# Optimization experiments

Hardware: AMD Instinct MI355X
Metric: run time of the kernel (lower is better)

The kernel has to match this reference:

```python
import jax, jax.numpy as jnp
import numpy as np

T, B, IN_DIM, MEM_DIM = 256, 64, 512, 512


def _kaiming(key, shape):
    # kaiming_normal_ default: fan_in = shape[1], gain = sqrt(2)
    std = np.sqrt(2.0 / shape[1])
    return jax.random.normal(key, shape, dtype=jnp.float32) * std


def setup_inputs() -> dict:
    key = jax.random.key(0)
    ks = jax.random.split(key, 10)
    inp = {
        "inputs": jax.random.normal(ks[0], (T, B, IN_DIM), dtype=jnp.float32),
        "emb_s": jax.random.normal(ks[1], (T, B, IN_DIM), dtype=jnp.float32),
        "c0": jnp.zeros((B, MEM_DIM), dtype=jnp.float32),
        "h0": jnp.zeros((B, MEM_DIM), dtype=jnp.float32),
        # learned params (torch Linear: y = x @ W.T + b)
        "W_ioux": _kaiming(ks[2], (4 * MEM_DIM, IN_DIM)),
        "b_ioux": jnp.zeros((4 * MEM_DIM,), jnp.float32),
        "W_iouh": _kaiming(ks[3], (4 * MEM_DIM, MEM_DIM)),
        "b_iouh": jnp.zeros((4 * MEM_DIM,), jnp.float32),
        "W_ious": _kaiming(ks[4], (4 * MEM_DIM, IN_DIM)),
        "b_ious": jnp.zeros((4 * MEM_DIM,), jnp.float32),
        "W_fx": _kaiming(ks[5], (MEM_DIM, IN_DIM)),
        "b_fx": jnp.zeros((MEM_DIM,), jnp.float32),
        "W_fh": _kaiming(ks[6], (MEM_DIM, MEM_DIM)),
        "b_fh": jnp.zeros((MEM_DIM,), jnp.float32),
        "W_wc": _kaiming(ks[7], (MEM_DIM, IN_DIM)),
        "b_wc": jnp.zeros((MEM_DIM,), jnp.float32),
    }
    return inp


def reference(inputs, emb_s, c0, h0,
              W_ioux, b_ioux, W_iouh, b_iouh, W_ious, b_ious,
              W_fx, b_fx, W_fh, b_fh, W_wc, b_wc):
    M = W_fh.shape[0]
    # Precompute all input-dependent projections for the whole sequence (big GEMMs).
    iou_x = (jnp.einsum('tbi,gi->tbg', inputs, W_ioux) + b_ioux
             + jnp.einsum('tbi,gi->tbg', emb_s, W_ious) + b_ious)      # [T,B,4M]
    ctelta_x = jnp.einsum('tbi,mi->tbm', inputs, W_fx) + b_fx          # [T,B,M]
    wc_s = jnp.tanh(jnp.einsum('tbi,mi->tbm', emb_s, W_wc) + b_wc)    # [T,B,M]

    def step(carry, xs):
        c, h = carry
        iou_t, ctx_t, wcs_t = xs
        iou = iou_t + h @ W_iouh.T + b_iouh                            # [B,4M]
        f, i, o, o_c = jnp.split(jax.nn.sigmoid(iou), 4, axis=1)
        c_telta = jnp.tanh(ctx_t + h @ W_fh.T + b_fh)
        c_new = i * c_telta + f * c
        h_new = o * jnp.tanh(c_new) + o_c * wcs_t
        return (c_new, h_new), h_new

    (c_fin, h_fin), out = jax.lax.scan(step, (c0, h0), (iou_x, ctelta_x, wc_s))
    return out, (c_fin, h_fin)
```

## Files before the change

### kernel.cpp

```cpp
#include <hip/hip_runtime.h>
#include <stdint.h>

#define T_STEPS 256
#define B_DIM   64
#define MDIM    512
#define NROWS   (T_STEPS * B_DIM)
#define KCAT    1024
#define NBIG    3072
#define W2ROWS  2560
#define NBLK2   32
#define OUT_N   ((size_t)T_STEPS * B_DIM * MDIM)

typedef short v8s __attribute__((ext_vector_type(8)));
typedef float v4f __attribute__((ext_vector_type(4)));
typedef unsigned long long u64;

static __device__ __forceinline__ unsigned short f2bf(float f) {
    unsigned u = __builtin_bit_cast(unsigned, f);
    u += 0x7FFFu + ((u >> 16) & 1u);
    return (unsigned short)(u >> 16);
}
static __device__ __forceinline__ float bf2f(unsigned short h) {
    unsigned u = ((unsigned)h) << 16;
    return __builtin_bit_cast(float, u);
}
static __device__ __forceinline__ float fast_rcp(float x) {
    return __builtin_amdgcn_rcpf(x);
}
static __device__ __forceinline__ float sigmoid_fast(float x) {
    return fast_rcp(1.0f + __expf(-x));
}
static __device__ __forceinline__ float tanh_fast(float x) {
    return 1.0f - 2.0f * fast_rcp(1.0f + __expf(2.0f * x));
}


__global__ void pack_xcat(const float* __restrict__ x, const float* __restrict__ s,
                          unsigned short* __restrict__ xcat) {
    int idx = blockIdx.x * blockDim.x + threadIdx.x;
    if (idx >= NROWS * KCAT) return;
    int row = idx >> 10, col = idx & 1023;
    float v = (col < 512) ? x[row * 512 + col] : s[row * 512 + (col - 512)];
    xcat[idx] = f2bf(v);
}

__global__ void pack_wbig(const float* __restrict__ Wioux, const float* __restrict__ bioux,
                          const float* __restrict__ Wious, const float* __restrict__ bious,
                          const float* __restrict__ Wfx,   const float* __restrict__ bfx,
                          const float* __restrict__ Wwc,   const float* __restrict__ bwc,
                          unsigned short* __restrict__ wbig, float* __restrict__ bbig) {
    int idx = blockIdx.x * blockDim.x + threadIdx.x;
    if (idx >= NBIG * KCAT) return;
    int r = idx >> 10, c = idx & 1023;
    float v;
    if (r < 2048)      v = (c < 512) ? Wioux[r * 512 + c] : Wious[r * 512 + (c - 512)];
    else if (r < 2560) { int j = r - 2048; v = (c < 512) ? Wfx[j * 512 + c] : 0.0f; }
    else               { int j = r - 2560; v = (c < 512) ? 0.0f : Wwc[j * 512 + (c - 512)]; }
    wbig[idx] = f2bf(v);
    if (c == 0) {
        float b;
        if (r < 2048)      b = bioux[r] + bious[r];
        else if (r < 2560) b = bfx[r - 2048];
        else               b = bwc[r - 2560];
        bbig[r] = b;
    }
}

__global__ void pack_w2(const float* __restrict__ Wiouh, const float* __restrict__ biouh,
                        const float* __restrict__ Wfh,   const float* __restrict__ bfh,
                        unsigned short* __restrict__ w2, float* __restrict__ b2) {
    int idx = blockIdx.x * blockDim.x + threadIdx.x;
    if (idx >= W2ROWS * 512) return;
    int r = idx >> 9, k = idx & 511;
    int bk = r / 80, rem = r % 80, g = rem >> 4, j = rem & 15;
    int m = bk * 16 + j;
    float v, bias;
    if (g < 4) { v = Wiouh[(size_t)(g * 512 + m) * 512 + k]; bias = biouh[g * 512 + m]; }
    else       { v = Wfh[(size_t)m * 512 + k];               bias = bfh[m]; }
    w2[idx] = f2bf(v);
    if (k == 0) b2[r] = bias;
}

__global__ void init_state(const float* __restrict__ h0,
                           unsigned short* __restrict__ hslab0,
                           int* __restrict__ flags) {
    int idx = blockIdx.x * blockDim.x + threadIdx.x;
    if (idx < 2048) flags[idx] = 0;
    if (idx >= B_DIM * MDIM) return;
    int row = idx >> 9, col = idx & 511;
    hslab0[((col >> 4) * 64 + row) * 16 + (col & 15)] = f2bf(h0[idx]);
}


__global__ __launch_bounds__(256) void gemm_big(
        const unsigned short* __restrict__ xcat,
        const unsigned short* __restrict__ wbig,
        const float* __restrict__ bbig,
        unsigned short* __restrict__ ytile) {
    __shared__ __align__(16) unsigned short As[128][40];
    __shared__ __align__(16) unsigned short Bs[128][40];
    int nb = blockIdx.x;
    int mb = blockIdx.y;
    int tid = threadIdx.x;
    int lane = tid & 63, wid = tid >> 6;
    int wm = wid & 1, wn = wid >> 1;
    int lm = lane & 15, lq = lane >> 4;
    v4f acc[4][4] = {};
    for (int kb = 0; kb < KCAT / 32; ++kb) {
        __syncthreads();
        #pragma unroll
        for (int it = 0; it < 2; ++it) {
            int cid = tid + it * 256;
            int r = cid >> 2, q = cid & 3;
            *(uint4*)&As[r][q * 8] =
                *(const uint4*)(xcat + (size_t)(mb * 128 + r) * KCAT + kb * 32 + q * 8);
            *(uint4*)&Bs[r][q * 8] =
                *(const uint4*)(wbig + (size_t)(nb * 128 + r) * KCAT + kb * 32 + q * 8);
        }
        __syncthreads();
        v8s a[4], b[4];
        #pragma unroll
        for (int i = 0; i < 4; ++i) a[i] = *(const v8s*)&As[wm * 64 + i * 16 + lm][lq * 8];
        #pragma unroll
        for (int j = 0; j < 4; ++j) b[j] = *(const v8s*)&Bs[wn * 64 + j * 16 + lm][lq * 8];
        #pragma unroll
        for (int i = 0; i < 4; ++i)
            #pragma unroll
            for (int j = 0; j < 4; ++j)
                acc[i][j] = __builtin_amdgcn_mfma_f32_16x16x32_bf16(a[i], b[j], acc[i][j], 0, 0, 0);
    }
    int tt = mb * 2 + wm;
    #pragma unroll
    for (int i = 0; i < 4; ++i) {
        int rbase = i * 16 + lq * 4;
        #pragma unroll
        for (int j = 0; j < 4; ++j) {
            int gn = nb * 128 + wn * 64 + j * 16 + lm;
            float bias = bbig[gn];
            bool do_tanh = (gn >= 2560);
            int slot, mcol;
            if (gn < 2048)      { slot = gn >> 9; mcol = gn & 511; }
            else if (gn < 2560) { slot = 4; mcol = gn - 2048; }
            else                { slot = 5; mcol = gn - 2560; }
            size_t base = ((((size_t)tt * NBLK2 + (mcol >> 4)) * 64 + rbase) * 6 + slot) * 16
                          + (mcol & 15);
            #pragma unroll
            for (int r = 0; r < 4; ++r) {
                float v = acc[i][j][r] + bias;
                if (do_tanh) v = tanhf(v);
                ytile[base + (size_t)r * 96] = f2bf(v);
            }
        }
    }
}


__global__ __launch_bounds__(256, 1) void lstm_persist(
        const unsigned short* __restrict__ ytile,
        const unsigned short* __restrict__ w2,
        const float* __restrict__ b2,
        const float* __restrict__ c0,
        unsigned short* hslab0,
        unsigned short* hslab1,
        float* __restrict__ out,
        int* __restrict__ flags) {
    __shared__ __align__(16) float red[2][10][256];
    __shared__ __align__(16) unsigned short ybuf[2][6144];
    int bk = blockIdx.x;
    int tid = threadIdx.x;
    int lane = tid & 63, wid = tid >> 6;
    int p = wid >> 1;
    int q = wid & 1;
    int lm = lane & 15, lq = lane >> 4;
    int m = bk * 16 + lm;

    v8s bfrag[5][8];
    const unsigned short* w2b = w2 + (size_t)(bk * 80 + lm) * 512 + lq * 8;
    #pragma unroll
    for (int g = 0; g < 5; ++g)
        #pragma unroll
        for (int j = 0; j < 8; ++j)
            bfrag[g][j] = *(const v8s*)(w2b + (size_t)g * 16 * 512 + (q * 8 + j) * 32);

    float bias[5];
    #pragma unroll
    for (int g = 0; g < 5; ++g) bias[g] = b2[(bk * 5 + g) * 16 + lm];
    float creg[2][4];
    #pragma unroll
    for (int tb = 0; tb < 2; ++tb)
        #pragma unroll
        for (int r = 0; r < 4; ++r)
            creg[tb][r] = c0[(p * 32 + tb * 16 + lq * 4 + r) * 512 + m];

    if (q == 1) {
        const unsigned short* slab = ytile + (size_t)bk * 6144;
        #pragma unroll
        for (int i = 0; i < 6; ++i) {
            int ch = p * 6 + i;
            __builtin_amdgcn_global_load_lds(
                (const __attribute__((address_space(1))) unsigned int*)(slab + ch * 512 + lane * 8),
                (__attribute__((address_space(3))) unsigned int*)(&ybuf[0][0] + ch * 512), 16, 0, 0);
        }
    }

    for (int t = 0; t < T_STEPS; ++t) {
        int cur = t & 1;
        if (t) {
            if (wid == 1)
                while (!__all(__hip_atomic_load(flags + lane * 32, __ATOMIC_RELAXED,
                                                __HIP_MEMORY_SCOPE_AGENT) >= t)) {}
            __syncthreads();
            asm volatile("" ::: "memory");
        }
        const u64* hin = cur ? (const u64*)hslab1 : (const u64*)hslab0;
        unsigned*  hnx = cur ? (unsigned*)hslab0 : (unsigned*)hslab1;
        u64 hq[32];
        {
            const u64* hb = hin + ((size_t)(q * 16 + (lq >> 1)) * 64 + p * 32 + lm) * 4
                          + (lq & 1) * 2;
            #pragma unroll
            for (int j = 0; j < 8; ++j) {
                hq[j * 4 + 0] = __hip_atomic_load(hb + j * 512,      __ATOMIC_RELAXED, __HIP_MEMORY_SCOPE_AGENT);
                hq[j * 4 + 1] = __hip_atomic_load(hb + j * 512 + 1,  __ATOMIC_RELAXED, __HIP_MEMORY_SCOPE_AGENT);
                hq[j * 4 + 2] = __hip_atomic_load(hb + j * 512 + 64, __ATOMIC_RELAXED, __HIP_MEMORY_SCOPE_AGENT);
                hq[j * 4 + 3] = __hip_atomic_load(hb + j * 512 + 65, __ATOMIC_RELAXED, __HIP_MEMORY_SCOPE_AGENT);
            }
        }
        v4f acc[2][5] = {};
        #pragma unroll
        for (int j = 0; j < 8; ++j) {
            union { u64 qq[2]; v8s v; } a0, a1;
            a0.qq[0] = hq[j * 4 + 0]; a0.qq[1] = hq[j * 4 + 1];
            a1.qq[0] = hq[j * 4 + 2]; a1.qq[1] = hq[j * 4 + 3];
            #pragma unroll
            for (int g = 0; g < 5; ++g) {
                acc[0][g] = __builtin_amdgcn_mfma_f32_16x16x32_bf16(a0.v, bfrag[g][j], acc[0][g], 0, 0, 0);
                acc[1][g] = __builtin_amdgcn_mfma_f32_16x16x32_bf16(a1.v, bfrag[g][j], acc[1][g], 0, 0, 0);
            }
        }
        if (q == 1) {
            #pragma unroll
            for (int tb = 0; tb < 2; ++tb)
                #pragma unroll
                for (int g = 0; g < 5; ++g)
                    *(v4f*)&red[p][tb * 5 + g][lane * 4] = acc[tb][g];
        }
        __syncthreads();
        if (q == 0) {
            #pragma unroll
            for (int tb = 0; tb < 2; ++tb)
                #pragma unroll
                for (int g = 0; g < 5; ++g)
                    acc[tb][g] += *(const v4f*)&red[p][tb * 5 + g][lane * 4];
            const unsigned short* yb = &ybuf[cur][0];
            float hnv[2][4];
            unsigned hbf[2][4];
            #pragma unroll
            for (int tb = 0; tb < 2; ++tb) {
                #pragma unroll
                for (int r = 0; r < 4; ++r) {
                    int brow = p * 32 + tb * 16 + lq * 4 + r;
                    const unsigned short* ybr = yb + brow * 96;
                    float f_ = sigmoid_fast(bf2f(ybr[0 * 16 + lm]) + acc[tb][0][r] + bias[0]);
                    float i_ = sigmoid_fast(bf2f(ybr[1 * 16 + lm]) + acc[tb][1][r] + bias[1]);
                    float o_ = sigmoid_fast(bf2f(ybr[2 * 16 + lm]) + acc[tb][2][r] + bias[2]);
                    float oc = sigmoid_fast(bf2f(ybr[3 * 16 + lm]) + acc[tb][3][r] + bias[3]);
                    float ct = tanh_fast  (bf2f(ybr[4 * 16 + lm]) + acc[tb][4][r] + bias[4]);
                    float wcs = bf2f(ybr[5 * 16 + lm]);
                    float cn = i_ * ct + f_ * creg[tb][r];
                    creg[tb][r] = cn;
                    float hn = o_ * tanh_fast(cn) + oc * wcs;
                    hnv[tb][r] = hn;
                    hbf[tb][r] = f2bf(hn);
                }
            }
            #pragma unroll
            for (int tb = 0; tb < 2; ++tb)
                #pragma unroll
                for (int r = 0; r < 4; ++r) {
                    int brow = p * 32 + tb * 16 + lq * 4 + r;
                    unsigned other = (unsigned)__shfl_xor((int)hbf[tb][r], 1);
                    if ((lm & 1) == 0) {
                        unsigned w = (hbf[tb][r] & 0xFFFFu) | (other << 16);
                        __hip_atomic_store(hnx + (size_t)(bk * 64 + brow) * 8 + (lm >> 1), w,
                                           __ATOMIC_RELAXED, __HIP_MEMORY_SCOPE_AGENT);
                    }
                }
            asm volatile("s_waitcnt vmcnt(0)" ::: "memory");
            if (lane == 0 && t + 1 < T_STEPS)
                __hip_atomic_store(flags + (bk * 2 + p) * 32, t + 1,
                                   __ATOMIC_RELAXED, __HIP_MEMORY_SCOPE_AGENT);
            #pragma unroll
            for (int tb = 0; tb < 2; ++tb)
                #pragma unroll
                for (int r = 0; r < 4; ++r) {
                    int brow = p * 32 + tb * 16 + lq * 4 + r;
                    out[((size_t)t * 64 + brow) * 512 + m] = hnv[tb][r];
                    if (t == T_STEPS - 1)
                        out[OUT_N + 32768 + (size_t)brow * 512 + m] = hnv[tb][r];
                }
        } else if (t + 1 < T_STEPS) {
            const unsigned short* slab = ytile + (size_t)((t + 1) * NBLK2 + bk) * 6144;
            unsigned short* lbase = &ybuf[cur ^ 1][0];
            #pragma unroll
            for (int i = 0; i < 6; ++i) {
                int ch = p * 6 + i;
                __builtin_amdgcn_global_load_lds(
                    (const __attribute__((address_space(1))) unsigned int*)(slab + ch * 512 + lane * 8),
                    (__attribute__((address_space(3))) unsigned int*)(lbase + ch * 512), 16, 0, 0);
            }
        }
    }

    if (q == 0) {
        #pragma unroll
        for (int tb = 0; tb < 2; ++tb)
            #pragma unroll
            for (int r = 0; r < 4; ++r)
                out[OUT_N + (size_t)(p * 32 + tb * 16 + lq * 4 + r) * 512 + m] = creg[tb][r];
    }
}


extern "C" void kernel_launch(void* const* d_in, const int* in_sizes, int n_in,
                              void* d_out, int out_size, void* d_ws, size_t ws_size,
                              hipStream_t stream) {
    const float* inputs = (const float*)d_in[0];
    const float* emb_s  = (const float*)d_in[1];
    const float* c0     = (const float*)d_in[2];
    const float* h0     = (const float*)d_in[3];
    const float* W_ioux = (const float*)d_in[4];  const float* b_ioux = (const float*)d_in[5];
    const float* W_iouh = (const float*)d_in[6];  const float* b_iouh = (const float*)d_in[7];
    const float* W_ious = (const float*)d_in[8];  const float* b_ious = (const float*)d_in[9];
    const float* W_fx   = (const float*)d_in[10]; const float* b_fx   = (const float*)d_in[11];
    const float* W_fh   = (const float*)d_in[12]; const float* b_fh   = (const float*)d_in[13];
    const float* W_wc   = (const float*)d_in[14]; const float* b_wc   = (const float*)d_in[15];
    float* out = (float*)d_out;

    char* ws = (char*)d_ws;
    size_t off = 0;
    auto alloc = [&](size_t bytes) -> void* {
        void* p = ws + off;
        off += (bytes + 255) & ~(size_t)255;
        return p;
    };
    unsigned short* ytile = (unsigned short*)alloc((size_t)NROWS * NBIG * 2);
    unsigned short* xcat  = (unsigned short*)alloc((size_t)NROWS * KCAT * 2);
    unsigned short* wbig  = (unsigned short*)alloc((size_t)NBIG * KCAT * 2);
    float*          bbig  = (float*)alloc(NBIG * 4);
    unsigned short* w2    = (unsigned short*)alloc((size_t)W2ROWS * 512 * 2);
    float*          b2    = (float*)alloc(W2ROWS * 4);
    unsigned short* hslab0 = (unsigned short*)alloc(B_DIM * MDIM * 2);
    unsigned short* hslab1 = (unsigned short*)alloc(B_DIM * MDIM * 2);
    int*            flags  = (int*)alloc(8192);

    pack_xcat<<<(NROWS * KCAT + 255) / 256, 256, 0, stream>>>(inputs, emb_s, xcat);
    pack_wbig<<<(NBIG * KCAT + 255) / 256, 256, 0, stream>>>(
        W_ioux, b_ioux, W_ious, b_ious, W_fx, b_fx, W_wc, b_wc, wbig, bbig);
    pack_w2<<<(W2ROWS * 512 + 255) / 256, 256, 0, stream>>>(W_iouh, b_iouh, W_fh, b_fh, w2, b2);
    init_state<<<(B_DIM * MDIM + 255) / 256, 256, 0, stream>>>(h0, hslab0, flags);

    dim3 g1(NBIG / 128, NROWS / 128);
    gemm_big<<<g1, 256, 0, stream>>>(xcat, wbig, bbig, ytile);

    lstm_persist<<<NBLK2, 256, 0, stream>>>(ytile, w2, b2, c0, hslab0, hslab1, out, flags);
}
```

Measured before the change: 1.884 ms.

## Replace flag barrier with per-element step tags on hidden-state words

The persistent LSTM kernel drops the separate flag array and spin barrier. Each hidden-state value is now stored as a 32-bit word carrying a bf16 value plus a step tag, and readers spin until every word they need carries the expected tag, so data and readiness arrive together. It also splits the gate epilogue across both wave halves instead of one, and uses a triple-buffered prefetch issued by all waves. The cost is twice the hidden-state traffic, repeated polling of 64 words per lane, and extra permute instructions to unpack the tagged words.

```diff
diff --git a/kernel.cpp b/kernel.cpp
--- a/kernel.cpp
+++ b/kernel.cpp
@@ -82,13 +82,12 @@
 }
 
 __global__ void init_state(const float* __restrict__ h0,
-                           unsigned short* __restrict__ hslab0,
-                           int* __restrict__ flags) {
+                           unsigned* __restrict__ hs0,
+                           unsigned* __restrict__ hs1) {
     int idx = blockIdx.x * blockDim.x + threadIdx.x;
-    if (idx < 2048) flags[idx] = 0;
     if (idx >= B_DIM * MDIM) return;
-    int row = idx >> 9, col = idx & 511;
-    hslab0[((col >> 4) * 64 + row) * 16 + (col & 15)] = f2bf(h0[idx]);
+    hs0[idx] = (unsigned)f2bf(h0[idx]);
+    hs1[idx] = 0xFFFF0000u;
 }
 
 
@@ -160,12 +159,11 @@
         const unsigned short* __restrict__ w2,
         const float* __restrict__ b2,
         const float* __restrict__ c0,
-        unsigned short* hslab0,
-        unsigned short* hslab1,
-        float* __restrict__ out,
-        int* __restrict__ flags) {
-    __shared__ __align__(16) float red[2][10][256];
-    __shared__ __align__(16) unsigned short ybuf[2][6144];
+        unsigned* hs0,
+        unsigned* hs1,
+        float* __restrict__ out) {
+    __shared__ __align__(16) float red[2][2][5][256];
+    __shared__ __align__(16) unsigned short ybuf[3][6144];
     int bk = blockIdx.x;
     int tid = threadIdx.x;
     int lane = tid & 63, wid = tid >> 6;
@@ -185,140 +183,112 @@
     float bias[5];
     #pragma unroll
     for (int g = 0; g < 5; ++g) bias[g] = b2[(bk * 5 + g) * 16 + lm];
-    float creg[2][4];
-    #pragma unroll
-    for (int tb = 0; tb < 2; ++tb)
-        #pragma unroll
-        for (int r = 0; r < 4; ++r)
-            creg[tb][r] = c0[(p * 32 + tb * 16 + lq * 4 + r) * 512 + m];
-
-    if (q == 1) {
-        const unsigned short* slab = ytile + (size_t)bk * 6144;
-        #pragma unroll
-        for (int i = 0; i < 6; ++i) {
-            int ch = p * 6 + i;
+    float creg[4];
+    #pragma unroll
+    for (int r = 0; r < 4; ++r)
+        creg[r] = c0[(p * 32 + q * 16 + lq * 4 + r) * 512 + m];
+
+    auto prefetch = [&](int tt, int buf) {
+        const unsigned short* slab = ytile + ((size_t)tt * NBLK2 + bk) * 6144;
+        unsigned short* lbase = &ybuf[buf][0];
+        #pragma unroll
+        for (int i = 0; i < 3; ++i) {
+            int ch = wid * 3 + i;
             __builtin_amdgcn_global_load_lds(
                 (const __attribute__((address_space(1))) unsigned int*)(slab + ch * 512 + lane * 8),
-                (__attribute__((address_space(3))) unsigned int*)(&ybuf[0][0] + ch * 512), 16, 0, 0);
-        }
-    }
+                (__attribute__((address_space(3))) unsigned int*)(lbase + ch * 512), 16, 0, 0);
+        }
+    };
+    prefetch(0, 0);
+    prefetch(1, 1);
 
     for (int t = 0; t < T_STEPS; ++t) {
-        int cur = t & 1;
-        if (t) {
-            if (wid == 1)
-                while (!__all(__hip_atomic_load(flags + lane * 32, __ATOMIC_RELAXED,
-                                                __HIP_MEMORY_SCOPE_AGENT) >= t)) {}
-            __syncthreads();
-            asm volatile("" ::: "memory");
-        }
-        const u64* hin = cur ? (const u64*)hslab1 : (const u64*)hslab0;
-        unsigned*  hnx = cur ? (unsigned*)hslab0 : (unsigned*)hslab1;
-        u64 hq[32];
+        const unsigned* hin = (t & 1) ? hs1 : hs0;
+        unsigned*       hnx = (t & 1) ? hs0 : hs1;
+        u64 wv[64];
         {
-            const u64* hb = hin + ((size_t)(q * 16 + (lq >> 1)) * 64 + p * 32 + lm) * 4
-                          + (lq & 1) * 2;
+            const u64* hb = (const u64*)hin + ((size_t)(p * 32 + lm)) * 256 + q * 128 + lq * 4;
+            unsigned tg = (unsigned)t & 0xFFFFu;
+            u64 ex = ((u64)tg << 16) | ((u64)tg << 48);
+            while (true) {
+                #pragma unroll
+                for (int j = 0; j < 8; ++j)
+                    #pragma unroll
+                    for (int e = 0; e < 4; ++e) {
+                        wv[j * 4 + e]      = __hip_atomic_load(hb + j * 16 + e,
+                                                __ATOMIC_RELAXED, __HIP_MEMORY_SCOPE_AGENT);
+                        wv[32 + j * 4 + e] = __hip_atomic_load(hb + 4096 + j * 16 + e,
+                                                __ATOMIC_RELAXED, __HIP_MEMORY_SCOPE_AGENT);
+                    }
+                bool ok = true;
+                #pragma unroll
+                for (int i = 0; i < 64; ++i)
+                    ok &= ((wv[i] & 0xFFFF0000FFFF0000ULL) == ex);
+                if (__all(ok)) break;
+            }
+        }
+        v8s a0[8], a1[8];
+        #pragma unroll
+        for (int j = 0; j < 8; ++j) {
+            union { unsigned u[4]; v8s v; } f0, f1;
             #pragma unroll
-            for (int j = 0; j < 8; ++j) {
-                hq[j * 4 + 0] = __hip_atomic_load(hb + j * 512,      __ATOMIC_RELAXED, __HIP_MEMORY_SCOPE_AGENT);
-                hq[j * 4 + 1] = __hip_atomic_load(hb + j * 512 + 1,  __ATOMIC_RELAXED, __HIP_MEMORY_SCOPE_AGENT);
-                hq[j * 4 + 2] = __hip_atomic_load(hb + j * 512 + 64, __ATOMIC_RELAXED, __HIP_MEMORY_SCOPE_AGENT);
-                hq[j * 4 + 3] = __hip_atomic_load(hb + j * 512 + 65, __ATOMIC_RELAXED, __HIP_MEMORY_SCOPE_AGENT);
+            for (int e = 0; e < 4; ++e) {
+                u64 x0 = wv[j * 4 + e], x1 = wv[32 + j * 4 + e];
+                f0.u[e] = __builtin_amdgcn_perm((unsigned)(x0 >> 32), (unsigned)x0, 0x05040100u);
+                f1.u[e] = __builtin_amdgcn_perm((unsigned)(x1 >> 32), (unsigned)x1, 0x05040100u);
             }
+            a0[j] = f0.v; a1[j] = f1.v;
         }
         v4f acc[2][5] = {};
         #pragma unroll
         for (int j = 0; j < 8; ++j) {
-            union { u64 qq[2]; v8s v; } a0, a1;
-            a0.qq[0] = hq[j * 4 + 0]; a0.qq[1] = hq[j * 4 + 1];
-            a1.qq[0] = hq[j * 4 + 2]; a1.qq[1] = hq[j * 4 + 3];
             #pragma unroll
             for (int g = 0; g < 5; ++g) {
-                acc[0][g] = __builtin_amdgcn_mfma_f32_16x16x32_bf16(a0.v, bfrag[g][j], acc[0][g], 0, 0, 0);
-                acc[1][g] = __builtin_amdgcn_mfma_f32_16x16x32_bf16(a1.v, bfrag[g][j], acc[1][g], 0, 0, 0);
+                acc[0][g] = __builtin_amdgcn_mfma_f32_16x16x32_bf16(a0[j], bfrag[g][j], acc[0][g], 0, 0, 0);
+                acc[1][g] = __builtin_amdgcn_mfma_f32_16x16x32_bf16(a1[j], bfrag[g][j], acc[1][g], 0, 0, 0);
             }
         }
-        if (q == 1) {
-            #pragma unroll
-            for (int tb = 0; tb < 2; ++tb)
-                #pragma unroll
-                for (int g = 0; g < 5; ++g)
-                    *(v4f*)&red[p][tb * 5 + g][lane * 4] = acc[tb][g];
-        }
+        #pragma unroll
+        for (int g = 0; g < 5; ++g)
+            *(v4f*)&red[p][q ^ 1][g][lane * 4] = acc[q ^ 1][g];
         __syncthreads();
-        if (q == 0) {
-            #pragma unroll
-            for (int tb = 0; tb < 2; ++tb)
-                #pragma unroll
-                for (int g = 0; g < 5; ++g)
-                    acc[tb][g] += *(const v4f*)&red[p][tb * 5 + g][lane * 4];
-            const unsigned short* yb = &ybuf[cur][0];
-            float hnv[2][4];
-            unsigned hbf[2][4];
-            #pragma unroll
-            for (int tb = 0; tb < 2; ++tb) {
-                #pragma unroll
-                for (int r = 0; r < 4; ++r) {
-                    int brow = p * 32 + tb * 16 + lq * 4 + r;
-                    const unsigned short* ybr = yb + brow * 96;
-                    float f_ = sigmoid_fast(bf2f(ybr[0 * 16 + lm]) + acc[tb][0][r] + bias[0]);
-                    float i_ = sigmoid_fast(bf2f(ybr[1 * 16 + lm]) + acc[tb][1][r] + bias[1]);
-                    float o_ = sigmoid_fast(bf2f(ybr[2 * 16 + lm]) + acc[tb][2][r] + bias[2]);
-                    float oc = sigmoid_fast(bf2f(ybr[3 * 16 + lm]) + acc[tb][3][r] + bias[3]);
-                    float ct = tanh_fast  (bf2f(ybr[4 * 16 + lm]) + acc[tb][4][r] + bias[4]);
-                    float wcs = bf2f(ybr[5 * 16 + lm]);
-                    float cn = i_ * ct + f_ * creg[tb][r];
-                    creg[tb][r] = cn;
-                    float hn = o_ * tanh_fast(cn) + oc * wcs;
-                    hnv[tb][r] = hn;
-                    hbf[tb][r] = f2bf(hn);
-                }
-            }
-            #pragma unroll
-            for (int tb = 0; tb < 2; ++tb)
-                #pragma unroll
-                for (int r = 0; r < 4; ++r) {
-                    int brow = p * 32 + tb * 16 + lq * 4 + r;
-                    unsigned other = (unsigned)__shfl_xor((int)hbf[tb][r], 1);
-                    if ((lm & 1) == 0) {
-                        unsigned w = (hbf[tb][r] & 0xFFFFu) | (other << 16);
-                        __hip_atomic_store(hnx + (size_t)(bk * 64 + brow) * 8 + (lm >> 1), w,
-                                           __ATOMIC_RELAXED, __HIP_MEMORY_SCOPE_AGENT);
-                    }
-                }
-            asm volatile("s_waitcnt vmcnt(0)" ::: "memory");
-            if (lane == 0 && t + 1 < T_STEPS)
-                __hip_atomic_store(flags + (bk * 2 + p) * 32, t + 1,
-                                   __ATOMIC_RELAXED, __HIP_MEMORY_SCOPE_AGENT);
-            #pragma unroll
-            for (int tb = 0; tb < 2; ++tb)
-                #pragma unroll
-                for (int r = 0; r < 4; ++r) {
-                    int brow = p * 32 + tb * 16 + lq * 4 + r;
-                    out[((size_t)t * 64 + brow) * 512 + m] = hnv[tb][r];
-                    if (t == T_STEPS - 1)
-                        out[OUT_N + 32768 + (size_t)brow * 512 + m] = hnv[tb][r];
-                }
-        } else if (t + 1 < T_STEPS) {
-            const unsigned short* slab = ytile + (size_t)((t + 1) * NBLK2 + bk) * 6144;
-            unsigned short* lbase = &ybuf[cur ^ 1][0];
-            #pragma unroll
-            for (int i = 0; i < 6; ++i) {
-                int ch = p * 6 + i;
-                __builtin_amdgcn_global_load_lds(
-                    (const __attribute__((address_space(1))) unsigned int*)(slab + ch * 512 + lane * 8),
-                    (__attribute__((address_space(3))) unsigned int*)(lbase + ch * 512), 16, 0, 0);
-            }
+        if (t + 2 < T_STEPS) prefetch(t + 2, (t + 2) % 3);
+        v4f fin[5];
+        #pragma unroll
+        for (int g = 0; g < 5; ++g)
+            fin[g] = acc[q][g] + *(const v4f*)&red[p][q][g][lane * 4];
+        const unsigned short* yb = &ybuf[t % 3][0];
+        unsigned tagup = ((unsigned)(t + 1)) << 16;
+        float hv[4];
+        #pragma unroll
+        for (int r = 0; r < 4; ++r) {
+            int brow = p * 32 + q * 16 + lq * 4 + r;
+            const unsigned short* ybr = yb + brow * 96;
+            float f_ = sigmoid_fast(bf2f(ybr[0 * 16 + lm]) + fin[0][r] + bias[0]);
+            float i_ = sigmoid_fast(bf2f(ybr[1 * 16 + lm]) + fin[1][r] + bias[1]);
+            float o_ = sigmoid_fast(bf2f(ybr[2 * 16 + lm]) + fin[2][r] + bias[2]);
+            float oc = sigmoid_fast(bf2f(ybr[3 * 16 + lm]) + fin[3][r] + bias[3]);
+            float ct = tanh_fast  (bf2f(ybr[4 * 16 + lm]) + fin[4][r] + bias[4]);
+            float wcs = bf2f(ybr[5 * 16 + lm]);
+            float cn = i_ * ct + f_ * creg[r];
+            creg[r] = cn;
+            float hn = o_ * tanh_fast(cn) + oc * wcs;
+            hv[r] = hn;
+            __hip_atomic_store(hnx + (size_t)brow * 512 + m, tagup | (unsigned)f2bf(hn),
+                               __ATOMIC_RELAXED, __HIP_MEMORY_SCOPE_AGENT);
+        }
+        #pragma unroll
+        for (int r = 0; r < 4; ++r) {
+            int brow = p * 32 + q * 16 + lq * 4 + r;
+            out[((size_t)t * 64 + brow) * 512 + m] = hv[r];
+            if (t == T_STEPS - 1)
+                out[OUT_N + 32768 + (size_t)brow * 512 + m] = hv[r];
         }
     }
 
-    if (q == 0) {
-        #pragma unroll
-        for (int tb = 0; tb < 2; ++tb)
-            #pragma unroll
-            for (int r = 0; r < 4; ++r)
-                out[OUT_N + (size_t)(p * 32 + tb * 16 + lq * 4 + r) * 512 + m] = creg[tb][r];
-    }
+    #pragma unroll
+    for (int r = 0; r < 4; ++r)
+        out[OUT_N + (size_t)(p * 32 + q * 16 + lq * 4 + r) * 512 + m] = creg[r];
 }
 
 
@@ -350,18 +320,17 @@
     float*          bbig  = (float*)alloc(NBIG * 4);
     unsigned short* w2    = (unsigned short*)alloc((size_t)W2ROWS * 512 * 2);
     float*          b2    = (float*)alloc(W2ROWS * 4);
-    unsigned short* hslab0 = (unsigned short*)alloc(B_DIM * MDIM * 2);
-    unsigned short* hslab1 = (unsigned short*)alloc(B_DIM * MDIM * 2);
-    int*            flags  = (int*)alloc(8192);
+    unsigned*       hs0   = (unsigned*)alloc((size_t)B_DIM * MDIM * 4);
+    unsigned*       hs1   = (unsigned*)alloc((size_t)B_DIM * MDIM * 4);
 
     pack_xcat<<<(NROWS * KCAT + 255) / 256, 256, 0, stream>>>(inputs, emb_s, xcat);
     pack_wbig<<<(NBIG * KCAT + 255) / 256, 256, 0, stream>>>(
         W_ioux, b_ioux, W_ious, b_ious, W_fx, b_fx, W_wc, b_wc, wbig, bbig);
     pack_w2<<<(W2ROWS * 512 + 255) / 256, 256, 0, stream>>>(W_iouh, b_iouh, W_fh, b_fh, w2, b2);
-    init_state<<<(B_DIM * MDIM + 255) / 256, 256, 0, stream>>>(h0, hslab0, flags);
+    init_state<<<(B_DIM * MDIM + 255) / 256, 256, 0, stream>>>(h0, hs0, hs1);
 
     dim3 g1(NBIG / 128, NROWS / 128);
     gemm_big<<<g1, 256, 0, stream>>>(xcat, wbig, bbig, ytile);
 
-    lstm_persist<<<NBLK2, 256, 0, stream>>>(ytile, w2, b2, c0, hslab0, hslab1, out, flags);
-}
+    lstm_persist<<<NBLK2, 256, 0, stream>>>(ytile, w2, b2, c0, hs0, hs1, out);
+}
```

After: 3.948 ms. 110% more time.
